# Kernel tuning notes

Hardware: AMD Instinct MI355X
Metric: run time of the kernel (lower is better)

Reference implementation:

```python
import jax, jax.numpy as jnp
import numpy as np

# Physical constants hardcoded in the torch module: m=[1.0, 50.0], l=[1.0, 1.0], g=10.0
M_DIAG = jnp.array([1.0, 1.0, 50.0, 50.0], dtype=jnp.float32)  # mass matrix diagonal [m0,m0,m1,m1]
G = 10.0


def _phi(x):
    # x: [4] = (x0, y0, x1, y1); two holonomic rod-length constraints
    c1 = x[0] ** 2 + x[1] ** 2 - 1.0
    c2 = (x[0] - x[2]) ** 2 + (x[1] - x[3]) ** 2 - 1.0
    return jnp.stack([c1, c2])  # [2]


def _potential(x):
    # U = sum_i m_i * g * y_i  (y coords are x[1], x[3])
    return M_DIAG[0] * G * x[1] + M_DIAG[2] * G * x[3]


def _forward(coords):
    x, v = jnp.split(coords, 2, axis=-1)  # each [bs, 4]
    minv = (1.0 / M_DIAG).astype(coords.dtype)  # diagonal of M^{-1}, [4]

    # phi_q[:, i] = d phi_i / dx  -> [bs, 2, 4]
    phi_q = jax.vmap(jax.jacfwd(_phi))(x)

    # phi_qq[:, i] = d/dx ( phi_q[i] . v )  -> [bs, 2, 4]
    def _gdot(xi, vi):
        return jax.jacfwd(_phi)(xi) @ vi  # [2]

    phi_qq = jax.vmap(jax.jacfwd(_gdot, argnums=0))(x, v)

    # F = -dV/dx  -> [bs, 4]
    F = -jax.vmap(jax.grad(_potential))(x)

    # Minv is diagonal: phi_q @ Minv == phi_q * minv (broadcast over last axis)
    phiq_Minv = phi_q * minv  # [bs, 2, 4]

    L = jnp.einsum('bik,bjk->bij', phiq_Minv, phi_q)  # [bs, 2, 2]
    R = jnp.einsum('bik,bk->bi', phiq_Minv, F) + jnp.einsum('bik,bk->bi', phi_qq, v)  # [bs, 2]
    lam = jnp.einsum('bij,bj->bi', jnp.linalg.inv(L), R)  # [bs, 2]

    a = minv * (F - jnp.einsum('bik,bi->bk', phi_q, lam))  # [bs, 4]
    return jnp.concatenate([v, a], axis=-1)  # [bs, 8]


def setup_inputs() -> dict:
    key = jax.random.key(0)
    coords = jax.random.normal(key, (2097152, 8), dtype=jnp.float32)
    t = jnp.zeros((1,), dtype=jnp.float32)
    return {"t": t, "coords": coords}


def reference(t, coords):
    # t is unused in the dynamics (autonomous system), matching the torch forward
    return _forward(coords)
```

## Files before the change

kernel.cpp:

```cpp
#include <hip/hip_runtime.h>


typedef float vfloat4_t __attribute__((ext_vector_type(4)));

#define UNROLL 8

__device__ __forceinline__ float4 pend2_process(float4 mine, bool odd) {
    float4 other;
    other.x = __shfl_xor(mine.x, 1);
    other.y = __shfl_xor(mine.y, 1);
    other.z = __shfl_xor(mine.z, 1);
    other.w = __shfl_xor(mine.w, 1);

    float4 p = odd ? other : mine;
    float4 q = odd ? mine : other;

    float x0 = p.x, y0 = p.y, x1 = p.z, y1 = p.w;
    float u0 = q.x, w0 = q.y, u1 = q.z, w1 = q.w;

    float dx = x0 - x1, dy = y0 - y1;
    float du = u0 - u1, dw = w0 - w1;

    float L11 = 4.0f * (x0 * x0 + y0 * y0);
    float L12 = 4.0f * (x0 * dx + y0 * dy);
    float L22 = 4.08f * (dx * dx + dy * dy);

    float R1 = -20.0f * y0 + 2.0f * (u0 * u0 + w0 * w0);
    float R2 = 2.0f * (du * du + dw * dw);

    float det = L11 * L22 - L12 * L12;
    float inv = 1.0f / det;
    float lam1 = (L22 * R1 - L12 * R2) * inv;
    float lam2 = (L11 * R2 - L12 * R1) * inv;

    float4 res;
    if (odd) {
        res.x = -2.0f * (x0 * lam1 + dx * lam2);
        res.y = -10.0f - 2.0f * (y0 * lam1 + dy * lam2);
        res.z = 0.04f * dx * lam2;
        res.w = -10.0f + 0.04f * dy * lam2;
    } else {
        res = q;
    }
    return res;
}

__global__ __launch_bounds__(256) void pend2_dae_kernel(
    const float4* __restrict__ in,
    float4* __restrict__ out,
    int n4)
{
    const int NT  = gridDim.x * blockDim.x;
    const int t   = blockIdx.x * blockDim.x + threadIdx.x;
    const bool odd = (t & 1);

    const int span  = NT * UNROLL;
    const int nfull = (n4 / span) * span;

    for (int base = 0; base < nfull; base += span) {
        float4 v[UNROLL];
        #pragma unroll
        for (int k = 0; k < UNROLL; ++k)
            v[k] = in[base + k * NT + t];

        #pragma unroll
        for (int k = 0; k < UNROLL; ++k) {
            float4 r = pend2_process(v[k], odd);
            out[base + k * NT + t] = r;
        }
    }

    for (int j = nfull + t; j < n4; j += NT) {
        float4 r = pend2_process(in[j], odd);
        out[j] = r;
    }
}

extern "C" void kernel_launch(void* const* d_in, const int* in_sizes, int n_in,
                              void* d_out, int out_size, void* d_ws, size_t ws_size,
                              hipStream_t stream) {
    const float4* coords = (const float4*)d_in[1];
    float4* out = (float4*)d_out;
    int n4 = in_sizes[1] / 4;

    int block = 256;
    long long want = ((long long)n4 + (long long)block * UNROLL - 1)
                     / ((long long)block * UNROLL);
    int grid = (int)(want < 1 ? 1 : (want > 2048 ? 2048 : want));
    pend2_dae_kernel<<<grid, block, 0, stream>>>(coords, out, n4);
}
```

Measured before the change: 118.7 us.

## Process one row per thread with nontemporal loads and stores, drop shuffles

Replaces the pairwise shuffle scheme, where two lanes shared a row, with one thread per 8-float row that loads both float4 halves directly. It also switches to nontemporal loads and stores and to a one-shot grid without a grid-stride loop or unroll. The aim is to remove cross-lane shuffles and the divergent odd/even paths and to bypass cache pollution on a streaming kernel. In exchange, each lane's two loads are strided by 32 bytes, so per-instruction coalescing is looser, and the many small blocks give up explicit memory-level parallelism from unrolling.

Result: slower. 133.3 us (+12.3%).

```diff
diff --git a/kernel.cpp b/kernel.cpp
--- a/kernel.cpp
+++ b/kernel.cpp
@@ -3,17 +3,16 @@
 
 typedef float vfloat4_t __attribute__((ext_vector_type(4)));
 
-#define UNROLL 8
+__global__ __launch_bounds__(256) void pend2_dae_kernel(
+    const vfloat4_t* __restrict__ in,
+    vfloat4_t* __restrict__ out,
+    int nrows)
+{
+    int r = blockIdx.x * blockDim.x + threadIdx.x;
+    if (r >= nrows) return;
 
-__device__ __forceinline__ float4 pend2_process(float4 mine, bool odd) {
-    float4 other;
-    other.x = __shfl_xor(mine.x, 1);
-    other.y = __shfl_xor(mine.y, 1);
-    other.z = __shfl_xor(mine.z, 1);
-    other.w = __shfl_xor(mine.w, 1);
-
-    float4 p = odd ? other : mine;
-    float4 q = odd ? mine : other;
+    vfloat4_t p = __builtin_nontemporal_load(&in[2 * r]);
+    vfloat4_t q = __builtin_nontemporal_load(&in[2 * r + 1]);
 
     float x0 = p.x, y0 = p.y, x1 = p.z, y1 = p.w;
     float u0 = q.x, w0 = q.y, u1 = q.z, w1 = q.w;
@@ -33,59 +32,24 @@
     float lam1 = (L22 * R1 - L12 * R2) * inv;
     float lam2 = (L11 * R2 - L12 * R1) * inv;
 
-    float4 res;
-    if (odd) {
-        res.x = -2.0f * (x0 * lam1 + dx * lam2);
-        res.y = -10.0f - 2.0f * (y0 * lam1 + dy * lam2);
-        res.z = 0.04f * dx * lam2;
-        res.w = -10.0f + 0.04f * dy * lam2;
-    } else {
-        res = q;
-    }
-    return res;
-}
+    vfloat4_t a;
+    a.x = -2.0f * (x0 * lam1 + dx * lam2);
+    a.y = -10.0f - 2.0f * (y0 * lam1 + dy * lam2);
+    a.z = 0.04f * dx * lam2;
+    a.w = -10.0f + 0.04f * dy * lam2;
 
-__global__ __launch_bounds__(256) void pend2_dae_kernel(
-    const float4* __restrict__ in,
-    float4* __restrict__ out,
-    int n4)
-{
-    const int NT  = gridDim.x * blockDim.x;
-    const int t   = blockIdx.x * blockDim.x + threadIdx.x;
-    const bool odd = (t & 1);
-
-    const int span  = NT * UNROLL;
-    const int nfull = (n4 / span) * span;
-
-    for (int base = 0; base < nfull; base += span) {
-        float4 v[UNROLL];
-        #pragma unroll
-        for (int k = 0; k < UNROLL; ++k)
-            v[k] = in[base + k * NT + t];
-
-        #pragma unroll
-        for (int k = 0; k < UNROLL; ++k) {
-            float4 r = pend2_process(v[k], odd);
-            out[base + k * NT + t] = r;
-        }
-    }
-
-    for (int j = nfull + t; j < n4; j += NT) {
-        float4 r = pend2_process(in[j], odd);
-        out[j] = r;
-    }
+    __builtin_nontemporal_store(q, &out[2 * r]);
+    __builtin_nontemporal_store(a, &out[2 * r + 1]);
 }
 
 extern "C" void kernel_launch(void* const* d_in, const int* in_sizes, int n_in,
                               void* d_out, int out_size, void* d_ws, size_t ws_size,
                               hipStream_t stream) {
-    const float4* coords = (const float4*)d_in[1];
-    float4* out = (float4*)d_out;
-    int n4 = in_sizes[1] / 4;
+    const vfloat4_t* coords = (const vfloat4_t*)d_in[1];
+    vfloat4_t* out = (vfloat4_t*)d_out;
+    int nrows = in_sizes[1] / 8;
 
     int block = 256;
-    long long want = ((long long)n4 + (long long)block * UNROLL - 1)
-                     / ((long long)block * UNROLL);
-    int grid = (int)(want < 1 ? 1 : (want > 2048 ? 2048 : want));
-    pend2_dae_kernel<<<grid, block, 0, stream>>>(coords, out, n4);
+    int grid = (nrows + block - 1) / block;
+    pend2_dae_kernel<<<grid, block, 0, stream>>>(coords, out, nrows);
 }
```
